# Optimization experiments

Hardware: AMD Instinct MI355X
Metric: run time of the kernel (lower is better)

Reference implementation:

```python
import jax, jax.numpy as jnp
import numpy as np
from jax import lax

C = 256          # hidden_channels
K_ITERS = 3      # num_iterations

def _conv(x, w, b, stride=1, pad='SAME'):
    y = lax.conv_general_dilated(x, w, (stride, stride), pad,
                                 dimension_numbers=('NCHW', 'OIHW', 'NCHW'))
    return y + b[None, :, None, None]

def setup_inputs() -> dict:
    key = jax.random.key(0)
    ks = jax.random.split(key, 16)
    B, N, H, W = 1, 3, 384, 384
    def p(k, sh, scale=None):
        if scale is None:
            scale = 1.0 / np.sqrt(np.prod(sh[1:]))
        return jax.random.normal(k, sh, jnp.float32) * scale
    z = lambda: jnp.zeros((C,), jnp.float32)
    return {
        'frames': jax.random.normal(ks[0], (B, N, 3, H, W), jnp.float32),
        'backbone_w': p(ks[1], (C, 3, 8, 8)), 'backbone_b': z(),
        'W_intra': p(ks[2], (C, C), scale=1.0 / C),
        'W_inter': p(ks[3], (C, C), scale=1.0 / C),
        'gate_w': p(ks[4], (C, C, 1, 1)), 'gate_b': z(),
        'Wz': p(ks[5], (C, 2 * C, 3, 3)), 'bz': z(),
        'Wr': p(ks[6], (C, 2 * C, 3, 3)), 'br': z(),
        'Wh': p(ks[7], (C, 2 * C, 3, 3)), 'bh': z(),
        'ro_w1': p(ks[8], (C, 2 * C, 3, 3)), 'ro_b1': z(),
        'ro_w2': p(ks[9], (1, C, 3, 3)), 'ro_b2': jnp.zeros((1,), jnp.float32),
    }

def _forward(frames, backbone_w, backbone_b, W_intra, W_inter, gate_w, gate_b,
             Wz, bz, Wr, br, Wh, bh, ro_w1, ro_b1, ro_w2, ro_b2):
    B, N, _, H, W = frames.shape
    x = frames.reshape(B * N, 3, H, W)
    # backbone: stride-8 conv + ReLU -> node embeddings v (B*N, C, Hf, Wf)
    v = jax.nn.relu(_conv(x, backbone_w, backbone_b, stride=8, pad='VALID'))
    Hf, Wf = v.shape[2], v.shape[3]
    P = Hf * Wf
    v = v.reshape(B, N, C, Hf, Wf)
    h = v
    idx = jnp.arange(N)
    for _ in range(K_ITERS):
        hp = h.reshape(B, N, C, P).transpose(0, 1, 3, 2)      # (B,N,P,C)
        # inter attention e_ij = h_i W h_j^T over all ordered pairs
        t = jnp.einsum('bipc,cd->bipd', hp, W_inter)
        e = jnp.einsum('bipd,bjqd->bijpq', t, hp)              # (B,N,N,P,P)
        # intra (loop-edge) attention on the diagonal, own weight
        ti = jnp.einsum('bipc,cd->bipd', hp, W_intra)
        e_intra = jnp.einsum('bipd,biqd->bipq', ti, hp)        # (B,N,P,P)
        e = e.at[:, idx, idx].set(e_intra)
        attn = jax.nn.softmax(e, axis=-1)
        m = jnp.einsum('bijpq,bjqc->bijpc', attn, hp)          # msg j->i (B,N,N,P,C)
        m = m.transpose(0, 1, 2, 4, 3).reshape(B * N * N, C, Hf, Wf)
        # gated aggregation: sigmoid(1x1 conv) gate, sum over senders j
        g = jax.nn.sigmoid(_conv(m, gate_w, gate_b))
        magg = (g * m).reshape(B, N, N, C, Hf, Wf).sum(axis=2).reshape(B * N, C, Hf, Wf)
        # ConvGRU update
        hflat = h.reshape(B * N, C, Hf, Wf)
        mh = jnp.concatenate([magg, hflat], axis=1)
        zg = jax.nn.sigmoid(_conv(mh, Wz, bz))
        rg = jax.nn.sigmoid(_conv(mh, Wr, br))
        hc = jnp.tanh(_conv(jnp.concatenate([magg, rg * hflat], axis=1), Wh, bh))
        h = ((1.0 - zg) * hflat + zg * hc).reshape(B, N, C, Hf, Wf)
    # read-out on concat(h, v)
    cat = jnp.concatenate([h, v], axis=2).reshape(B * N, 2 * C, Hf, Wf)
    y = jax.nn.relu(_conv(cat, ro_w1, ro_b1))
    masks = _conv(y, ro_w2, ro_b2)
    return masks.reshape(B, N, 1, Hf, Wf)

def reference(frames, backbone_w, backbone_b, W_intra, W_inter, gate_w, gate_b,
              Wz, bz, Wr, br, Wh, bh, ro_w1, ro_b1, ro_w2, ro_b2):
    return _forward(frames, backbone_w, backbone_b, W_intra, W_inter, gate_w, gate_b,
                    Wz, bz, Wr, br, Wh, bh, ro_w1, ro_b1, ro_w2, ro_b2)
```

## Files before the change

kernel.cpp:

```cpp
#include <hip/hip_runtime.h>
#include <hip/hip_bf16.h>
#include <math.h>

#define PIX 2304
#define CCH 256
#define CP  589824
#define NCP 1769472
#define KC  4608
#define PADR 2512

typedef __hip_bfloat16 bf16;
typedef __attribute__((ext_vector_type(8))) short bf16x8;
typedef __attribute__((ext_vector_type(4))) float f32x4;

__device__ __forceinline__ float sigmoidf_(float x){ return 1.f/(1.f+__expf(-x)); }

__device__ __forceinline__ void gl_lds16(const bf16* g, bf16* lds){
    __builtin_amdgcn_global_load_lds(
        (const __attribute__((address_space(1))) void*)g,
        (__attribute__((address_space(3))) void*)lds, 16, 0, 0);
}
#define FENCE() asm volatile("" ::: "memory")

__device__ __forceinline__ float bperm_f(int srcLane, float v){
    return __int_as_float(__builtin_amdgcn_ds_bpermute(srcLane<<2, __float_as_int(v)));
}
__device__ __forceinline__ unsigned packbf(float lo, float hi){
    bf16 a = __float2bfloat16(lo), b = __float2bfloat16(hi);
    return (unsigned)(*(unsigned short*)&a) | ((unsigned)(*(unsigned short*)&b)<<16);
}

__global__ __launch_bounds__(384) void fattn_k(
    const bf16* __restrict__ T, const bf16* __restrict__ Ti,
    const bf16* __restrict__ Khp, const bf16* __restrict__ Vcp,
    bf16* __restrict__ Ob)
{
    __shared__ bf16 Ks[128*256];
    __shared__ bf16 Vs[256*128];
    __shared__ unsigned Ps[6][1024];
    const int z = blockIdx.z, i = z/3, j = z%3;
    const bf16* Q  = ((i==j)? Ti : T) + (long)i*CP;
    const bf16* Kp = Khp + (long)j*CP;
    const bf16* Vp = Vcp + (long)j*CP;
    const int tid = threadIdx.x, l = tid & 63, w = tid >> 6;
    const int g = l>>4, m = l&15;
    const int q0 = blockIdx.x*96;

    bf16x8 qf[8];
    {
        const bf16* qr = Q + (long)(q0 + w*16 + m)*256 + g*8;
        #pragma unroll
        for (int ks=0; ks<8; ++ks) qf[ks] = *(const bf16x8*)(qr + ks*32);
    }
    f32x4 oacc[16];
    #pragma unroll
    for (int nf=0; nf<16; ++nf) oacc[nf] = (f32x4){0.f,0.f,0.f,0.f};
    float mrun = -3e38f;
    float lrun = 0.f;

    auto stageK = [&](int t){
        const int kq = t*128;
        #pragma unroll
        for (int u=0; u<11; ++u){
            int idx = u*384 + tid;
            if (idx < 4096){
                int rr = idx>>5, cc = idx&31;
                gl_lds16(Kp + (long)(kq+rr)*256 + ((cc ^ (rr&7))<<3),
                         &Ks[(u*384 + (tid & ~63))*8]);
            }
        }
    };
    auto stageV = [&](int t){
        const int kq = t*128;
        #pragma unroll
        for (int u=0; u<11; ++u){
            int idx = u*384 + tid;
            if (idx < 4096){
                int rr = idx>>4, cc = idx&15;
                gl_lds16(Vp + (long)rr*2304 + kq + ((cc ^ (rr&7))<<3),
                         &Vs[(u*384 + (tid & ~63))*8]);
            }
        }
    };

    stageK(0); stageV(0);
    char* pw = (char*)&Ps[w][0];
    for (int t=0; t<18; ++t){
        asm volatile("s_waitcnt vmcnt(10)" ::: "memory");
        __builtin_amdgcn_s_barrier();
        FENCE();

        f32x4 sacc[8];
        #pragma unroll
        for (int nf=0; nf<8; ++nf) sacc[nf] = (f32x4){0.f,0.f,0.f,0.f};
        __builtin_amdgcn_s_setprio(1);
        #pragma unroll
        for (int ks=0; ks<8; ++ks){
            #pragma unroll
            for (int nf=0; nf<8; ++nf){
                int row = nf*16 + m;
                int phys = (ks*4 + g) ^ (row&7);
                bf16x8 kf = *(const bf16x8*)&Ks[row*256 + phys*8];
                sacc[nf] = __builtin_amdgcn_mfma_f32_16x16x32_bf16(kf, qf[ks], sacc[nf], 0,0,0);
            }
        }
        __builtin_amdgcn_s_setprio(0);
        FENCE();
        __builtin_amdgcn_s_barrier();
        FENCE();
        if (t+1 < 18) stageK(t+1);

        float pmax = -3e38f;
        #pragma unroll
        for (int nf=0; nf<8; ++nf)
            #pragma unroll
            for (int r=0; r<4; ++r) pmax = fmaxf(pmax, sacc[nf][r]);
        pmax = fmaxf(pmax, __shfl_xor(pmax, 16));
        pmax = fmaxf(pmax, __shfl_xor(pmax, 32));
        if (!__all(pmax - mrun <= 8.f)){
            float mn = fmaxf(mrun, pmax);
            float al = __expf(mrun - mn);
            mrun = mn;
            lrun *= al;
            float ar[4];
            #pragma unroll
            for (int r=0; r<4; ++r) ar[r] = bperm_f((l & 48) | (g*4 + r), al);
            #pragma unroll
            for (int nf=0; nf<16; ++nf)
                #pragma unroll
                for (int r=0; r<4; ++r) oacc[nf][r] *= ar[r];
        }
        float rs = 0.f;
        unsigned pk[8][2];
        #pragma unroll
        for (int nf=0; nf<8; ++nf){
            float p0 = __expf(sacc[nf][0] - mrun);
            float p1 = __expf(sacc[nf][1] - mrun);
            float p2 = __expf(sacc[nf][2] - mrun);
            float p3 = __expf(sacc[nf][3] - mrun);
            rs += (p0+p1) + (p2+p3);
            pk[nf][0] = packbf(p0, p1);
            pk[nf][1] = packbf(p2, p3);
        }
        rs += __shfl_xor(rs, 16);
        rs += __shfl_xor(rs, 32);
        lrun += rs;
        #pragma unroll
        for (int nf=0; nf<8; ++nf)
            #pragma unroll
            for (int s=0; s<2; ++s){
                int ba = m*256 + ((nf*32 + g*8 + s*4) ^ ((m&7)<<4));
                *(unsigned*)(pw + ba) = pk[nf][s];
            }
        asm volatile("s_waitcnt lgkmcnt(0)" ::: "memory");
        __builtin_amdgcn_sched_barrier(0);

        if (t+1 < 18) asm volatile("s_waitcnt vmcnt(10)" ::: "memory");
        else          asm volatile("s_waitcnt vmcnt(0)"  ::: "memory");
        __builtin_amdgcn_s_barrier();
        FENCE();

        __builtin_amdgcn_s_setprio(1);
        #pragma unroll
        for (int ks2=0; ks2<4; ++ks2){
            bf16x8 pa = *(const bf16x8*)(pw + m*256 + ((ks2*64 + g*16) ^ ((m&7)<<4)));
            #pragma unroll
            for (int nf=0; nf<16; ++nf){
                int row = nf*16 + m;
                int phys = (ks2*4 + g) ^ (row&7);
                bf16x8 bv = *(const bf16x8*)&Vs[row*128 + phys*8];
                oacc[nf] = __builtin_amdgcn_mfma_f32_16x16x32_bf16(pa, bv, oacc[nf], 0,0,0);
            }
        }
        __builtin_amdgcn_s_setprio(0);
        FENCE();
        __builtin_amdgcn_s_barrier();
        FENCE();
        if (t+1 < 18) stageV(t+1);
    }

    float linv = 1.f / lrun;
    float li[4];
    #pragma unroll
    for (int r=0; r<4; ++r) li[r] = bperm_f((l & 48) | (g*4 + r), linv);
    bf16* ob = Ob + (long)z*CP;
    const int prow0 = q0 + w*16 + g*4;
    #pragma unroll
    for (int nf=0; nf<16; ++nf){
        int c = nf*16 + m;
        #pragma unroll
        for (int r=0; r<4; ++r)
            ob[(long)(prow0+r)*256 + c] = __float2bfloat16(oacc[nf][r]*li[r]);
    }
}

template<int BN>
__global__ __launch_bounds__(256) void mgemm_k(
    const bf16* __restrict__ A0, const bf16* __restrict__ B, bf16* __restrict__ ob,
    int M, int lda, int ldb, int ldc,
    long bsB, long bsC, int nzJ, int Ksub)
{
    __shared__ bf16 As[2][128*64];
    __shared__ bf16 Bs[2][BN*64];
    const int jz = blockIdx.z % nzJ;
    const bf16* Ap = A0 + (long)blockIdx.x*128*lda;
    const bf16* Bp = B + jz*bsB + (long)blockIdx.y*BN*ldb;
    const int tid = threadIdx.x, l = tid & 63;
    const int wvu = tid & ~63;
    const int wr = tid>>7, wc = (tid>>6)&1;
    constexpr int NF = BN/32;
    f32x4 acc[4][NF];
    #pragma unroll
    for (int i=0;i<4;++i)
        #pragma unroll
        for (int j=0;j<NF;++j) acc[i][j] = (f32x4){0.f,0.f,0.f,0.f};

    auto stage = [&](int buf, int kb){
        #pragma unroll
        for (int u=0;u<4;++u){
            int idx = u*256 + tid;
            int row = idx>>3, g = (idx&7) ^ (row&7);
            gl_lds16(Ap + (long)row*lda + kb + g*8, &As[buf][(u*256+wvu)*8]);
        }
        #pragma unroll
        for (int u=0;u<BN/32;++u){
            int idx = u*256 + tid;
            int row = idx>>3, g = (idx&7) ^ (row&7);
            gl_lds16(Bp + (long)row*ldb + kb + g*8, &Bs[buf][(u*256+wvu)*8]);
        }
    };

    const int nk = Ksub >> 6;
    stage(0, 0);
    int cur = 0;
    for (int t=0; t<nk; ++t){
        if (t+1 < nk){
            stage(cur^1, (t+1)*64);
            if constexpr (BN==64) asm volatile("s_waitcnt vmcnt(6)" ::: "memory");
            else                  asm volatile("s_waitcnt vmcnt(8)" ::: "memory");
        } else {
            asm volatile("s_waitcnt vmcnt(0)" ::: "memory");
        }
        __builtin_amdgcn_s_barrier();
        FENCE();
        #pragma unroll
        for (int ks=0; ks<64; ks+=32){
            bf16x8 af[4], bfr[NF];
            #pragma unroll
            for (int i=0;i<4;++i){
                int row = wr*64 + i*16 + (l&15);
                af[i] = *(const bf16x8*)&As[cur][row*64 + ((((ks>>3)+(l>>4)) ^ (row&7))<<3)];
            }
            #pragma unroll
            for (int j=0;j<NF;++j){
                int row = wc*(BN/2) + j*16 + (l&15);
                bfr[j] = *(const bf16x8*)&Bs[cur][row*64 + ((((ks>>3)+(l>>4)) ^ (row&7))<<3)];
            }
            #pragma unroll
            for (int i=0;i<4;++i)
                #pragma unroll
                for (int j=0;j<NF;++j)
                    acc[i][j] = __builtin_amdgcn_mfma_f32_16x16x32_bf16(af[i], bfr[j], acc[i][j], 0,0,0);
        }
        FENCE();
        __builtin_amdgcn_s_barrier();
        FENCE();
        cur ^= 1;
    }

    const int mb = blockIdx.x*128 + wr*64, nb = blockIdx.y*BN + wc*(BN/2);
    #pragma unroll
    for (int i=0;i<4;++i)
        #pragma unroll
        for (int j=0;j<NF;++j){
            int gm0 = mb + i*16 + ((l>>4)<<2);
            int gn  = nb + j*16 + (l&15);
            #pragma unroll
            for (int r=0;r<4;++r)
                ob[jz*bsC + (long)(gm0+r)*ldc + gn] = __float2bfloat16(acc[i][j][r]);
        }
}

__global__ __launch_bounds__(256) void gatemm_k(
    const bf16* __restrict__ gatew, const bf16* __restrict__ Mb9,
    const float* __restrict__ gb, bf16* __restrict__ inpad)
{
    __shared__ bf16 As[2][128*64];
    __shared__ bf16 Bs[2][64*64];
    __shared__ bf16 Ts[64*136];
    const int tid = threadIdx.x, l = tid & 63, wvu = tid & ~63;
    const int wr = tid>>7, wc = (tid>>6)&1;
    const int i = blockIdx.z;
    const bf16* Ap = gatew + (long)blockIdx.x*128*256;
    const int nb0 = blockIdx.y*64;
    f32x4 msum[4][2];
    #pragma unroll
    for (int a=0;a<4;++a){ msum[a][0]=(f32x4){0,0,0,0}; msum[a][1]=(f32x4){0,0,0,0}; }

    for (int j=0; j<3; ++j){
        const bf16* Bp = Mb9 + (long)(i*3+j)*CP + (long)nb0*256;
        f32x4 acc[4][2];
        #pragma unroll
        for (int a=0;a<4;++a){ acc[a][0]=(f32x4){0,0,0,0}; acc[a][1]=(f32x4){0,0,0,0}; }
        auto stage = [&](int buf, int kb){
            #pragma unroll
            for (int u=0;u<4;++u){
                int idx = u*256 + tid;
                int row = idx>>3, g = (idx&7) ^ (row&7);
                gl_lds16(Ap + (long)row*256 + kb + g*8, &As[buf][(u*256+wvu)*8]);
            }
            #pragma unroll
            for (int u=0;u<2;++u){
                int idx = u*256 + tid;
                int row = idx>>3, g = (idx&7) ^ (row&7);
                gl_lds16(Bp + (long)row*256 + kb + g*8, &Bs[buf][(u*256+wvu)*8]);
            }
        };
        stage(0, 0);
        int cur = 0;
        for (int t=0; t<4; ++t){
            if (t+1 < 4){
                stage(cur^1, (t+1)*64);
                asm volatile("s_waitcnt vmcnt(6)" ::: "memory");
            } else {
                asm volatile("s_waitcnt vmcnt(0)" ::: "memory");
            }
            __builtin_amdgcn_s_barrier();
            FENCE();
            #pragma unroll
            for (int ks=0; ks<64; ks+=32){
                bf16x8 af[4], bfr[2];
                #pragma unroll
                for (int a=0;a<4;++a){
                    int row = wr*64 + a*16 + (l&15);
                    af[a] = *(const bf16x8*)&As[cur][row*64 + ((((ks>>3)+(l>>4)) ^ (row&7))<<3)];
                }
                #pragma unroll
                for (int b=0;b<2;++b){
                    int row = wc*32 + b*16 + (l&15);
                    bfr[b] = *(const bf16x8*)&Bs[cur][row*64 + ((((ks>>3)+(l>>4)) ^ (row&7))<<3)];
                }
                #pragma unroll
                for (int a=0;a<4;++a)
                    #pragma unroll
                    for (int b=0;b<2;++b)
                        acc[a][b] = __builtin_amdgcn_mfma_f32_16x16x32_bf16(af[a], bfr[b], acc[a][b], 0,0,0);
            }
            FENCE();
            __builtin_amdgcn_s_barrier();
            FENCE();
            cur ^= 1;
        }
        const bf16* mbz = Mb9 + (long)(i*3+j)*CP;
        const int mb = blockIdx.x*128 + wr*64;
        #pragma unroll
        for (int a=0;a<4;++a)
            #pragma unroll
            for (int b=0;b<2;++b){
                int gm0 = mb + a*16 + ((l>>4)<<2);
                int gn  = nb0 + wc*32 + b*16 + (l&15);
                #pragma unroll
                for (int r=0;r<4;++r){
                    int gm = gm0 + r;
                    float g = sigmoidf_(acc[a][b][r] + gb[gm]);
                    float mv = __bfloat162float(mbz[(long)gn*256 + gm]);
                    msum[a][b][r] += g*mv;
                }
            }
    }
    __syncthreads();
    const int mbl = wr*64;
    #pragma unroll
    for (int a=0;a<4;++a)
        #pragma unroll
        for (int b=0;b<2;++b){
            int cl0 = mbl + a*16 + ((l>>4)<<2);
            int pl  = wc*32 + b*16 + (l&15);
            #pragma unroll
            for (int r=0;r<4;++r)
                Ts[pl*136 + cl0 + r] = __float2bfloat16(msum[a][b][r]);
        }
    __syncthreads();
    const int pl = tid >> 2, seg = tid & 3;
    int p = nb0 + pl;
    int prow = p + 2*(p/48) + 51;
    bf16* dst = inpad + (long)i*PADR*512 + (long)prow*512 + blockIdx.x*128 + seg*32;
    #pragma unroll
    for (int k2=0; k2<4; ++k2)
        *(uint4*)(dst + k2*8) = *(const uint4*)&Ts[pl*136 + seg*32 + k2*8];
}

__global__ __launch_bounds__(256) void cgemm2_k(
    const bf16* __restrict__ inpad, const bf16* __restrict__ W,
    float* __restrict__ part, int N)
{
    __shared__ bf16 As[2][128*64];
    __shared__ bf16 Bs[2][128*64];
    const int tid = threadIdx.x, l = tid & 63, wvu = tid & ~63;
    const int wr = tid>>7, wc = (tid>>6)&1;
    const int bx = blockIdx.x, by = blockIdx.y, kc = blockIdx.z;
    const int img = bx/18, m0 = (bx - img*18)*128;
    const bf16* Ab = inpad + (long)img*PADR*512;
    const bf16* Bb = W + (long)by*128*KC;
    f32x4 acc[4][4];
    #pragma unroll
    for (int i=0;i<4;++i)
        #pragma unroll
        for (int j=0;j<4;++j) acc[i][j] = (f32x4){0.f,0.f,0.f,0.f};

    auto stageA = [&](int buf, int k0){
        int tap = k0 >> 9, ci0 = k0 & 511;
        int dy = tap/3, dx = tap - 3*dy;
        int shift = (dy-1)*50 + (dx-1);
        #pragma unroll
        for (int u=0;u<4;++u){
            int idx = u*256 + tid;
            int row = idx>>3;
            int om = m0 + row;
            int prow = om + 2*(om/48) + 51 + shift;
            int g = (idx&7) ^ (row&7);
            gl_lds16(Ab + (long)prow*512 + ci0 + g*8, &As[buf][(u*256+wvu)*8]);
        }
    };
    auto stageB = [&](int buf, int k0){
        #pragma unroll
        for (int u=0;u<4;++u){
            int idx = u*256 + tid;
            int row = idx>>3;
            int g = (idx&7) ^ (row&7);
            gl_lds16(Bb + (long)row*KC + k0 + g*8, &Bs[buf][(u*256+wvu)*8]);
        }
    };

    const int kbeg = kc*2304;
    stageA(0, kbeg); stageB(0, kbeg);
    int cur = 0;
    for (int t=0; t<36; ++t){
        if (t+1 < 36){
            stageA(cur^1, kbeg+(t+1)*64); stageB(cur^1, kbeg+(t+1)*64);
            asm volatile("s_waitcnt vmcnt(8)" ::: "memory");
        } else {
            asm volatile("s_waitcnt vmcnt(0)" ::: "memory");
        }
        __builtin_amdgcn_s_barrier();
        FENCE();
        #pragma unroll
        for (int ks=0; ks<64; ks+=32){
            bf16x8 af[4], bfr[4];
            #pragma unroll
            for (int i=0;i<4;++i){
                int row = wr*64 + i*16 + (l&15);
                af[i] = *(const bf16x8*)&As[cur][row*64 + ((((ks>>3)+(l>>4)) ^ (row&7))<<3)];
            }
            #pragma unroll
            for (int j=0;j<4;++j){
                int row = wc*64 + j*16 + (l&15);
                bfr[j] = *(const bf16x8*)&Bs[cur][row*64 + ((((ks>>3)+(l>>4)) ^ (row&7))<<3)];
            }
            #pragma unroll
            for (int i=0;i<4;++i)
                #pragma unroll
                for (int j=0;j<4;++j)
                    acc[i][j] = __builtin_amdgcn_mfma_f32_16x16x32_bf16(af[i], bfr[j], acc[i][j], 0,0,0);
        }
        FENCE();
        __builtin_amdgcn_s_barrier();
        FENCE();
        cur ^= 1;
    }

    float* pbase = part + (long)kc*N*6912 + (long)img*2304;
    #pragma unroll
    for (int i=0;i<4;++i)
        #pragma unroll
        for (int j=0;j<4;++j){
            int gm0 = m0 + wr*64 + i*16 + ((l>>4)<<2);
            int gn  = by*128 + wc*64 + j*16 + (l&15);
            *(f32x4*)&pbase[(long)gn*6912 + gm0] = acc[i][j];
        }
}

__global__ __launch_bounds__(256) void credzr_k(const float* __restrict__ part,
        const float* __restrict__ bz, const float* __restrict__ br,
        const float* __restrict__ h, float* __restrict__ zg, bf16* __restrict__ inpad)
{
    __shared__ float tz[64][65];
    const int img = blockIdx.z, p0 = blockIdx.x*64, c0 = blockIdx.y*64;
    const int t = threadIdx.x, tx = t&63, tq = t>>6;
    #pragma unroll
    for (int u=0;u<16;++u){
        int cl = tq + u*4, c = c0 + cl;
        long pz = (long)c*6912 + (long)img*2304 + p0 + tx;
        float vz = part[pz] + part[pz + 512L*6912];
        long pr = (long)(c+256)*6912 + (long)img*2304 + p0 + tx;
        float vr = part[pr] + part[pr + 512L*6912];
        long hidx = (long)img*CP + (long)c*PIX + p0 + tx;
        float hv = h[hidx];
        zg[hidx] = sigmoidf_(vz + bz[c]);
        tz[cl][tx] = sigmoidf_(vr + br[c]) * hv;
    }
    __syncthreads();
    #pragma unroll
    for (int u=0;u<16;++u){
        int pl = tq + u*4, p = p0 + pl;
        int prow = p + 2*(p/48) + 51;
        inpad[(long)img*PADR*512 + (long)prow*512 + 256 + c0 + tx] = __float2bfloat16(tz[tx][pl]);
    }
}

__global__ __launch_bounds__(256) void credht_k(const float* __restrict__ part,
        const float* __restrict__ bh, const float* __restrict__ zg,
        float* __restrict__ h, bf16* __restrict__ hcp, bf16* __restrict__ hp,
        bf16* __restrict__ inpad)
{
    __shared__ float th[64][65];
    const int img = blockIdx.z, p0 = blockIdx.x*64, c0 = blockIdx.y*64;
    const int t = threadIdx.x, tx = t&63, tq = t>>6;
    #pragma unroll
    for (int u=0;u<16;++u){
        int cl = tq + u*4, c = c0 + cl;
        long pidx = (long)c*6912 + (long)img*2304 + p0 + tx;
        float vv = part[pidx] + part[pidx + 256L*6912];
        float hc = tanhf(vv + bh[c]);
        long hidx = (long)img*CP + (long)c*PIX + p0 + tx;
        float zv = zg[hidx];
        float hn = (1.f - zv)*h[hidx] + zv*hc;
        h[hidx] = hn;
        hcp[hidx] = __float2bfloat16(hn);
        th[cl][tx] = hn;
    }
    __syncthreads();
    #pragma unroll
    for (int u=0;u<16;++u){
        int pl = tq + u*4, p = p0 + pl;
        float val = th[tx][pl];
        hp[(long)img*CP + (long)p*256 + c0 + tx] = __float2bfloat16(val);
        int prow = p + 2*(p/48) + 51;
        inpad[(long)img*PADR*512 + (long)prow*512 + 256 + c0 + tx] = __float2bfloat16(val);
    }
}

__global__ __launch_bounds__(256) void credro_k(const float* __restrict__ part,
        const float* __restrict__ b0, float* __restrict__ o0)
{
    int id = blockIdx.x*256 + threadIdx.x;
    int c = id / 6912, g = id - c*6912;
    int img = g / 2304, p = g - img*2304;
    float v = part[id] + part[id + 256L*6912];
    o0[(long)img*CP + (long)c*PIX + p] = fmaxf(v + b0[c], 0.f);
}

__global__ __launch_bounds__(256) void padtr_k(const float* __restrict__ src,
        bf16* __restrict__ dst, int cofs)
{
    __shared__ float tile[64][65];
    const int img = blockIdx.z, p0 = blockIdx.x*64, c0 = blockIdx.y*64;
    const int t = threadIdx.x, tx = t&63, tq = t>>6;
    #pragma unroll
    for (int u=0;u<16;++u){
        int r = tq + u*4;
        tile[r][tx] = src[(long)img*CP + (long)(c0+r)*PIX + p0 + tx];
    }
    __syncthreads();
    bf16* d = dst + (long)img*PADR*512 + cofs + c0;
    #pragma unroll
    for (int u=0;u<16;++u){
        int pl = tq + u*4;
        int p = p0 + pl;
        int prow = p + 2*(p/48) + 51;
        d[(long)prow*512 + tx] = __float2bfloat16(tile[tx][pl]);
    }
}

__global__ __launch_bounds__(256) void convw_k(const float* __restrict__ src,
        bf16* __restrict__ dst, int total)
{
    int idx = blockIdx.x*256 + threadIdx.x;
    if (idx >= total) return;
    int co = idx / KC, r = idx - co*KC;
    int tap = r >> 9, ci = r & 511;
    dst[idx] = __float2bfloat16(src[(long)co*KC + ci*9 + tap]);
}

__global__ __launch_bounds__(256) void prep_h_k(const float* __restrict__ h,
        bf16* __restrict__ hcp, bf16* __restrict__ hp)
{
    __shared__ float tile[64][65];
    const int i = blockIdx.z, p0 = blockIdx.x*64, c0 = blockIdx.y*64;
    const int t = threadIdx.x, tx = t&63, tq = t>>6;
    #pragma unroll
    for (int s=0;s<16;++s){
        int r = tq + s*4;
        float v = h[(long)i*CP + (long)(c0+r)*PIX + p0 + tx];
        tile[r][tx] = v;
        hcp[(long)i*CP + (long)(c0+r)*PIX + p0 + tx] = __float2bfloat16(v);
    }
    __syncthreads();
    #pragma unroll
    for (int s=0;s<16;++s){
        int r = tq + s*4;
        hp[(long)i*CP + (long)(p0+r)*256 + c0 + tx] = __float2bfloat16(tile[tx][r]);
    }
}

__global__ __launch_bounds__(256) void convert_w_k(const float* __restrict__ wint,
    const float* __restrict__ wintra, const float* __restrict__ gw, bf16* __restrict__ o)
{
    int t = blockIdx.x*256 + threadIdx.x;
    int d = t >> 8, c = t & 255;
    o[t]          = __float2bfloat16(wint[c*256 + d]);
    o[65536 + t]  = __float2bfloat16(wintra[c*256 + d]);
    o[131072 + t] = __float2bfloat16(gw[t]);
}

__global__ __launch_bounds__(256) void backbone_k(
    const float* __restrict__ frames, const float* __restrict__ W,
    const float* __restrict__ bias, float* __restrict__ v, float* __restrict__ h)
{
    __shared__ float wl[3*64*4];
    const int n = blockIdx.z, o0 = blockIdx.y * 4;
    const int p = blockIdx.x * 256 + threadIdx.x;
    const int y = p / 48, x = p % 48;
    for (int e = threadIdx.x; e < 768; e += 256) {
        int o_sel = e / 192, rem = e % 192, ci = rem / 64, k = rem % 64;
        wl[(ci*64 + k)*4 + o_sel] = W[((long)(o0 + o_sel)*3 + ci)*64 + k];
    }
    __syncthreads();
    float acc[4] = {0.f,0.f,0.f,0.f};
    for (int ci = 0; ci < 3; ++ci) {
        const float* src = frames + (((long)n*3 + ci)*384) * 384;
        #pragma unroll
        for (int k = 0; k < 64; ++k) {
            int ky = k >> 3, kx = k & 7;
            float iv = src[(8*y + ky)*384 + 8*x + kx];
            float4 w = ((const float4*)wl)[ci*64 + k];
            acc[0] += iv*w.x; acc[1] += iv*w.y; acc[2] += iv*w.z; acc[3] += iv*w.w;
        }
    }
    #pragma unroll
    for (int oo = 0; oo < 4; ++oo) {
        float r = fmaxf(acc[oo] + bias[o0 + oo], 0.f);
        long idx = ((long)n*CCH + o0 + oo)*PIX + p;
        v[idx] = r; h[idx] = r;
    }
}

__global__ __launch_bounds__(256) void maskpart_k(const float* __restrict__ yin,
        const float* __restrict__ W, float* __restrict__ part)
{
    __shared__ float wl[288];
    const int cb = blockIdx.y * 32;
    for (int e = threadIdx.x; e < 288; e += 256) wl[e] = W[cb*9 + e];
    __syncthreads();
    int id = blockIdx.x*256 + threadIdx.x;
    int n = id / PIX, p = id - n*PIX;
    int y = p / 48, x = p % 48;
    float acc = 0.f;
    for (int ci = 0; ci < 32; ++ci) {
        const float* src = yin + ((long)n*CCH + cb + ci)*PIX;
        #pragma unroll
        for (int dy = 0; dy < 3; ++dy) {
            int yy = y + dy - 1;
            #pragma unroll
            for (int dx = 0; dx < 3; ++dx) {
                int xx = x + dx - 1;
                float iv = (yy >= 0 && yy < 48 && xx >= 0 && xx < 48) ? src[yy*48 + xx] : 0.f;
                acc += iv * wl[ci*9 + dy*3 + dx];
            }
        }
    }
    part[(long)blockIdx.y*(3*PIX) + id] = acc;
}

__global__ __launch_bounds__(256) void maskred_k(const float* __restrict__ part,
        const float* __restrict__ bias, float* __restrict__ out)
{
    int id = blockIdx.x*256 + threadIdx.x;
    float acc = bias[0];
    #pragma unroll
    for (int s = 0; s < 8; ++s) acc += part[(long)s*(3*PIX) + id];
    out[id] = acc;
}

extern "C" void kernel_launch(void* const* d_in, const int* in_sizes, int n_in,
                              void* d_out, int out_size, void* d_ws, size_t ws_size,
                              hipStream_t stream)
{
    const float* frames     = (const float*)d_in[0];
    const float* backbone_w = (const float*)d_in[1];
    const float* backbone_b = (const float*)d_in[2];
    const float* W_intra    = (const float*)d_in[3];
    const float* W_inter    = (const float*)d_in[4];
    const float* gate_w     = (const float*)d_in[5];
    const float* gate_b     = (const float*)d_in[6];
    const float* Wz         = (const float*)d_in[7];
    const float* bz         = (const float*)d_in[8];
    const float* Wr         = (const float*)d_in[9];
    const float* br         = (const float*)d_in[10];
    const float* Wh         = (const float*)d_in[11];
    const float* bh         = (const float*)d_in[12];
    const float* ro_w1      = (const float*)d_in[13];
    const float* ro_b1      = (const float*)d_in[14];
    const float* ro_w2      = (const float*)d_in[15];
    const float* ro_b2      = (const float*)d_in[16];
    float* out = (float*)d_out;
    float* ws  = (float*)d_ws;

    float* h    = ws + 0L*NCP;
    float* v    = ws + 1L*NCP;
    float* zg   = ws + 3L*NCP;
    float* S    = ws + 7L*NCP;

    float* Mb9f   = S;
    float* hp16f  = S + 7962624;
    float* hcp16f = hp16f + 884736;
    float* t16f   = hcp16f + 884736;
    float* ti16f  = t16f + 884736;
    float* wbase  = S + 11501568;
    bf16* Wint_t   = (bf16*)wbase;
    bf16* Wintra_t = Wint_t + 65536;
    bf16* gatew16  = Wint_t + 131072;
    bf16* cw16     = (bf16*)(wbase + 98304);
    bf16* inpad    = (bf16*)(wbase + 98304 + 2359296);
    float* maskp   = wbase + 98304 + 2359296 + 1929216;

    bf16* Mb9    = (bf16*)Mb9f;
    bf16* hp16   = (bf16*)hp16f;
    bf16* hcp16  = (bf16*)hcp16f;
    bf16* t16    = (bf16*)t16f;
    bf16* ti16   = (bf16*)ti16f;
    float* cpart = Mb9f;

    dim3 b256(256);

    hipMemsetAsync(inpad, 0, 3858432*sizeof(bf16), stream);
    backbone_k<<<dim3(9,64,3), b256, 0, stream>>>(frames, backbone_w, backbone_b, v, h);
    convert_w_k<<<dim3(256), b256, 0, stream>>>(W_inter, W_intra, gate_w, Wint_t);
    convw_k<<<dim3(4608), b256, 0, stream>>>(Wz, cw16, 256*KC);
    convw_k<<<dim3(4608), b256, 0, stream>>>(Wr, cw16 + 256L*KC, 256*KC);
    convw_k<<<dim3(4608), b256, 0, stream>>>(Wh, cw16 + 512L*KC, 256*KC);
    convw_k<<<dim3(4608), b256, 0, stream>>>(ro_w1, cw16 + 768L*KC, 256*KC);

    prep_h_k<<<dim3(36,4,3), b256, 0, stream>>>(h, hcp16, hp16);
    padtr_k<<<dim3(36,4,3), b256, 0, stream>>>(h, inpad, 256);

    for (int it = 0; it < 3; ++it) {
        mgemm_k<64><<<dim3(54,4,2), b256, 0, stream>>>(hp16, Wint_t, t16,
            6912, 256,256,256, 65536L, 1769472L, 2, 256);
        fattn_k<<<dim3(24,1,9), dim3(384), 0, stream>>>(t16, ti16, hp16, hcp16, Mb9);
        gatemm_k<<<dim3(2,36,3), b256, 0, stream>>>(gatew16, Mb9, gate_b, inpad);
        cgemm2_k<<<dim3(54,4,2), b256, 0, stream>>>(inpad, cw16, cpart, 512);
        credzr_k<<<dim3(36,4,3), b256, 0, stream>>>(cpart, bz, br, h, zg, inpad);
        cgemm2_k<<<dim3(54,2,2), b256, 0, stream>>>(inpad, cw16 + 512L*KC, cpart, 256);
        credht_k<<<dim3(36,4,3), b256, 0, stream>>>(cpart, bh, zg, h, hcp16, hp16, inpad);
    }

    padtr_k<<<dim3(36,4,3), b256, 0, stream>>>(h, inpad, 0);
    padtr_k<<<dim3(36,4,3), b256, 0, stream>>>(v, inpad, 256);
    cgemm2_k<<<dim3(54,2,2), b256, 0, stream>>>(inpad, cw16 + 768L*KC, cpart, 256);
    credro_k<<<dim3(6912), b256, 0, stream>>>(cpart, ro_b1, zg);
    maskpart_k<<<dim3(27,8), b256, 0, stream>>>(zg, ro_w2, maskp);
    maskred_k<<<dim3(27), b256, 0, stream>>>(maskp, ro_b2, out);
}
```

Before: 844.0 us.

## Process two query tiles per wave in flash attention, halving waves per block

```diff
diff --git a/kernel.cpp b/kernel.cpp
--- a/kernel.cpp
+++ b/kernel.cpp
@@ -30,7 +30,7 @@
     return (unsigned)(*(unsigned short*)&a) | ((unsigned)(*(unsigned short*)&b)<<16);
 }
 
-__global__ __launch_bounds__(384) void fattn_k(
+__global__ __launch_bounds__(192) void fattn_k(
     const bf16* __restrict__ T, const bf16* __restrict__ Ti,
     const bf16* __restrict__ Khp, const bf16* __restrict__ Vcp,
     bf16* __restrict__ Ob)
@@ -44,55 +44,66 @@
     const bf16* Vp = Vcp + (long)j*CP;
     const int tid = threadIdx.x, l = tid & 63, w = tid >> 6;
     const int g = l>>4, m = l&15;
-    const int q0 = blockIdx.x*96;
-
-    bf16x8 qf[8];
+    const int q0 = blockIdx.x*96 + w*32;
+
+    bf16x8 qf0[8], qf1[8];
     {
-        const bf16* qr = Q + (long)(q0 + w*16 + m)*256 + g*8;
-        #pragma unroll
-        for (int ks=0; ks<8; ++ks) qf[ks] = *(const bf16x8*)(qr + ks*32);
-    }
-    f32x4 oacc[16];
-    #pragma unroll
-    for (int nf=0; nf<16; ++nf) oacc[nf] = (f32x4){0.f,0.f,0.f,0.f};
-    float mrun = -3e38f;
-    float lrun = 0.f;
+        const bf16* qr0 = Q + (long)(q0 + m)*256 + g*8;
+        const bf16* qr1 = Q + (long)(q0 + 16 + m)*256 + g*8;
+        #pragma unroll
+        for (int ks=0; ks<8; ++ks){
+            qf0[ks] = *(const bf16x8*)(qr0 + ks*32);
+            qf1[ks] = *(const bf16x8*)(qr1 + ks*32);
+        }
+    }
+    f32x4 oacc0[16], oacc1[16];
+    #pragma unroll
+    for (int nf=0; nf<16; ++nf){
+        oacc0[nf] = (f32x4){0.f,0.f,0.f,0.f};
+        oacc1[nf] = (f32x4){0.f,0.f,0.f,0.f};
+    }
+    float mrun0 = -3e38f, lrun0 = 0.f;
+    float mrun1 = -3e38f, lrun1 = 0.f;
 
     auto stageK = [&](int t){
         const int kq = t*128;
         #pragma unroll
-        for (int u=0; u<11; ++u){
-            int idx = u*384 + tid;
+        for (int u=0; u<22; ++u){
+            int idx = u*192 + tid;
             if (idx < 4096){
                 int rr = idx>>5, cc = idx&31;
                 gl_lds16(Kp + (long)(kq+rr)*256 + ((cc ^ (rr&7))<<3),
-                         &Ks[(u*384 + (tid & ~63))*8]);
+                         &Ks[(u*192 + (tid & ~63))*8]);
             }
         }
     };
     auto stageV = [&](int t){
         const int kq = t*128;
         #pragma unroll
-        for (int u=0; u<11; ++u){
-            int idx = u*384 + tid;
+        for (int u=0; u<22; ++u){
+            int idx = u*192 + tid;
             if (idx < 4096){
                 int rr = idx>>4, cc = idx&15;
                 gl_lds16(Vp + (long)rr*2304 + kq + ((cc ^ (rr&7))<<3),
-                         &Vs[(u*384 + (tid & ~63))*8]);
+                         &Vs[(u*192 + (tid & ~63))*8]);
             }
         }
     };
 
     stageK(0); stageV(0);
-    char* pw = (char*)&Ps[w][0];
+    char* pw0 = (char*)Ps + (w*2+0)*4096;
+    char* pw1 = (char*)Ps + (w*2+1)*4096;
     for (int t=0; t<18; ++t){
-        asm volatile("s_waitcnt vmcnt(10)" ::: "memory");
+        asm volatile("s_waitcnt vmcnt(21)" ::: "memory");
         __builtin_amdgcn_s_barrier();
         FENCE();
 
-        f32x4 sacc[8];
-        #pragma unroll
-        for (int nf=0; nf<8; ++nf) sacc[nf] = (f32x4){0.f,0.f,0.f,0.f};
+        f32x4 sacc0[8], sacc1[8];
+        #pragma unroll
+        for (int nf=0; nf<8; ++nf){
+            sacc0[nf] = (f32x4){0.f,0.f,0.f,0.f};
+            sacc1[nf] = (f32x4){0.f,0.f,0.f,0.f};
+        }
         __builtin_amdgcn_s_setprio(1);
         #pragma unroll
         for (int ks=0; ks<8; ++ks){
@@ -101,7 +112,8 @@
                 int row = nf*16 + m;
                 int phys = (ks*4 + g) ^ (row&7);
                 bf16x8 kf = *(const bf16x8*)&Ks[row*256 + phys*8];
-                sacc[nf] = __builtin_amdgcn_mfma_f32_16x16x32_bf16(kf, qf[ks], sacc[nf], 0,0,0);
+                sacc0[nf] = __builtin_amdgcn_mfma_f32_16x16x32_bf16(kf, qf0[ks], sacc0[nf], 0,0,0);
+                sacc1[nf] = __builtin_amdgcn_mfma_f32_16x16x32_bf16(kf, qf1[ks], sacc1[nf], 0,0,0);
             }
         }
         __builtin_amdgcn_s_setprio(0);
@@ -110,52 +122,88 @@
         FENCE();
         if (t+1 < 18) stageK(t+1);
 
-        float pmax = -3e38f;
-        #pragma unroll
-        for (int nf=0; nf<8; ++nf)
-            #pragma unroll
-            for (int r=0; r<4; ++r) pmax = fmaxf(pmax, sacc[nf][r]);
-        pmax = fmaxf(pmax, __shfl_xor(pmax, 16));
-        pmax = fmaxf(pmax, __shfl_xor(pmax, 32));
-        if (!__all(pmax - mrun <= 8.f)){
-            float mn = fmaxf(mrun, pmax);
-            float al = __expf(mrun - mn);
-            mrun = mn;
-            lrun *= al;
-            float ar[4];
-            #pragma unroll
-            for (int r=0; r<4; ++r) ar[r] = bperm_f((l & 48) | (g*4 + r), al);
-            #pragma unroll
-            for (int nf=0; nf<16; ++nf)
-                #pragma unroll
-                for (int r=0; r<4; ++r) oacc[nf][r] *= ar[r];
-        }
-        float rs = 0.f;
-        unsigned pk[8][2];
-        #pragma unroll
-        for (int nf=0; nf<8; ++nf){
-            float p0 = __expf(sacc[nf][0] - mrun);
-            float p1 = __expf(sacc[nf][1] - mrun);
-            float p2 = __expf(sacc[nf][2] - mrun);
-            float p3 = __expf(sacc[nf][3] - mrun);
-            rs += (p0+p1) + (p2+p3);
-            pk[nf][0] = packbf(p0, p1);
-            pk[nf][1] = packbf(p2, p3);
-        }
-        rs += __shfl_xor(rs, 16);
-        rs += __shfl_xor(rs, 32);
-        lrun += rs;
-        #pragma unroll
-        for (int nf=0; nf<8; ++nf)
-            #pragma unroll
-            for (int s=0; s<2; ++s){
-                int ba = m*256 + ((nf*32 + g*8 + s*4) ^ ((m&7)<<4));
-                *(unsigned*)(pw + ba) = pk[nf][s];
-            }
+        {
+            float pmax = -3e38f;
+            #pragma unroll
+            for (int nf=0; nf<8; ++nf)
+                #pragma unroll
+                for (int r=0; r<4; ++r) pmax = fmaxf(pmax, sacc0[nf][r]);
+            pmax = fmaxf(pmax, __shfl_xor(pmax, 16));
+            pmax = fmaxf(pmax, __shfl_xor(pmax, 32));
+            if (!__all(pmax - mrun0 <= 8.f)){
+                float mn = fmaxf(mrun0, pmax);
+                float al = __expf(mrun0 - mn);
+                mrun0 = mn;
+                lrun0 *= al;
+                float ar[4];
+                #pragma unroll
+                for (int r=0; r<4; ++r) ar[r] = bperm_f((l & 48) | (g*4 + r), al);
+                #pragma unroll
+                for (int nf=0; nf<16; ++nf)
+                    #pragma unroll
+                    for (int r=0; r<4; ++r) oacc0[nf][r] *= ar[r];
+            }
+            float rs = 0.f;
+            #pragma unroll
+            for (int nf=0; nf<8; ++nf){
+                float p0 = __expf(sacc0[nf][0] - mrun0);
+                float p1 = __expf(sacc0[nf][1] - mrun0);
+                float p2 = __expf(sacc0[nf][2] - mrun0);
+                float p3 = __expf(sacc0[nf][3] - mrun0);
+                rs += (p0+p1) + (p2+p3);
+                unsigned k0 = packbf(p0, p1), k1 = packbf(p2, p3);
+                int ba0 = m*256 + ((nf*32 + g*8 + 0) ^ ((m&7)<<4));
+                int ba1 = m*256 + ((nf*32 + g*8 + 4) ^ ((m&7)<<4));
+                *(unsigned*)(pw0 + ba0) = k0;
+                *(unsigned*)(pw0 + ba1) = k1;
+            }
+            rs += __shfl_xor(rs, 16);
+            rs += __shfl_xor(rs, 32);
+            lrun0 += rs;
+        }
+        {
+            float pmax = -3e38f;
+            #pragma unroll
+            for (int nf=0; nf<8; ++nf)
+                #pragma unroll
+                for (int r=0; r<4; ++r) pmax = fmaxf(pmax, sacc1[nf][r]);
+            pmax = fmaxf(pmax, __shfl_xor(pmax, 16));
+            pmax = fmaxf(pmax, __shfl_xor(pmax, 32));
+            if (!__all(pmax - mrun1 <= 8.f)){
+                float mn = fmaxf(mrun1, pmax);
+                float al = __expf(mrun1 - mn);
+                mrun1 = mn;
+                lrun1 *= al;
+                float ar[4];
+                #pragma unroll
+                for (int r=0; r<4; ++r) ar[r] = bperm_f((l & 48) | (g*4 + r), al);
+                #pragma unroll
+                for (int nf=0; nf<16; ++nf)
+                    #pragma unroll
+                    for (int r=0; r<4; ++r) oacc1[nf][r] *= ar[r];
+            }
+            float rs = 0.f;
+            #pragma unroll
+            for (int nf=0; nf<8; ++nf){
+                float p0 = __expf(sacc1[nf][0] - mrun1);
+                float p1 = __expf(sacc1[nf][1] - mrun1);
+                float p2 = __expf(sacc1[nf][2] - mrun1);
+                float p3 = __expf(sacc1[nf][3] - mrun1);
+                rs += (p0+p1) + (p2+p3);
+                unsigned k0 = packbf(p0, p1), k1 = packbf(p2, p3);
+                int ba0 = m*256 + ((nf*32 + g*8 + 0) ^ ((m&7)<<4));
+                int ba1 = m*256 + ((nf*32 + g*8 + 4) ^ ((m&7)<<4));
+                *(unsigned*)(pw1 + ba0) = k0;
+                *(unsigned*)(pw1 + ba1) = k1;
+            }
+            rs += __shfl_xor(rs, 16);
+            rs += __shfl_xor(rs, 32);
+            lrun1 += rs;
+        }
         asm volatile("s_waitcnt lgkmcnt(0)" ::: "memory");
         __builtin_amdgcn_sched_barrier(0);
 
-        if (t+1 < 18) asm volatile("s_waitcnt vmcnt(10)" ::: "memory");
+        if (t+1 < 18) asm volatile("s_waitcnt vmcnt(21)" ::: "memory");
         else          asm volatile("s_waitcnt vmcnt(0)"  ::: "memory");
         __builtin_amdgcn_s_barrier();
         FENCE();
@@ -163,13 +211,15 @@
         __builtin_amdgcn_s_setprio(1);
         #pragma unroll
         for (int ks2=0; ks2<4; ++ks2){
-            bf16x8 pa = *(const bf16x8*)(pw + m*256 + ((ks2*64 + g*16) ^ ((m&7)<<4)));
+            bf16x8 pa0 = *(const bf16x8*)(pw0 + m*256 + ((ks2*64 + g*16) ^ ((m&7)<<4)));
+            bf16x8 pa1 = *(const bf16x8*)(pw1 + m*256 + ((ks2*64 + g*16) ^ ((m&7)<<4)));
             #pragma unroll
             for (int nf=0; nf<16; ++nf){
                 int row = nf*16 + m;
                 int phys = (ks2*4 + g) ^ (row&7);
                 bf16x8 bv = *(const bf16x8*)&Vs[row*128 + phys*8];
-                oacc[nf] = __builtin_amdgcn_mfma_f32_16x16x32_bf16(pa, bv, oacc[nf], 0,0,0);
+                oacc0[nf] = __builtin_amdgcn_mfma_f32_16x16x32_bf16(pa0, bv, oacc0[nf], 0,0,0);
+                oacc1[nf] = __builtin_amdgcn_mfma_f32_16x16x32_bf16(pa1, bv, oacc1[nf], 0,0,0);
             }
         }
         __builtin_amdgcn_s_setprio(0);
@@ -179,18 +229,34 @@
         if (t+1 < 18) stageV(t+1);
     }
 
-    float linv = 1.f / lrun;
-    float li[4];
-    #pragma unroll
-    for (int r=0; r<4; ++r) li[r] = bperm_f((l & 48) | (g*4 + r), linv);
     bf16* ob = Ob + (long)z*CP;
-    const int prow0 = q0 + w*16 + g*4;
-    #pragma unroll
-    for (int nf=0; nf<16; ++nf){
-        int c = nf*16 + m;
-        #pragma unroll
-        for (int r=0; r<4; ++r)
-            ob[(long)(prow0+r)*256 + c] = __float2bfloat16(oacc[nf][r]*li[r]);
+    {
+        float linv = 1.f / lrun0;
+        float li[4];
+        #pragma unroll
+        for (int r=0; r<4; ++r) li[r] = bperm_f((l & 48) | (g*4 + r), linv);
+        const int prow0 = q0 + g*4;
+        #pragma unroll
+        for (int nf=0; nf<16; ++nf){
+            int c = nf*16 + m;
+            #pragma unroll
+            for (int r=0; r<4; ++r)
+                ob[(long)(prow0+r)*256 + c] = __float2bfloat16(oacc0[nf][r]*li[r]);
+        }
+    }
+    {
+        float linv = 1.f / lrun1;
+        float li[4];
+        #pragma unroll
+        for (int r=0; r<4; ++r) li[r] = bperm_f((l & 48) | (g*4 + r), linv);
+        const int prow0 = q0 + 16 + g*4;
+        #pragma unroll
+        for (int nf=0; nf<16; ++nf){
+            int c = nf*16 + m;
+            #pragma unroll
+            for (int r=0; r<4; ++r)
+                ob[(long)(prow0+r)*256 + c] = __float2bfloat16(oacc1[nf][r]*li[r]);
+        }
     }
 }
 
@@ -747,7 +813,7 @@
     for (int it = 0; it < 3; ++it) {
         mgemm_k<64><<<dim3(54,4,2), b256, 0, stream>>>(hp16, Wint_t, t16,
             6912, 256,256,256, 65536L, 1769472L, 2, 256);
-        fattn_k<<<dim3(24,1,9), dim3(384), 0, stream>>>(t16, ti16, hp16, hcp16, Mb9);
+        fattn_k<<<dim3(24,1,9), dim3(192), 0, stream>>>(t16, ti16, hp16, hcp16, Mb9);
         gatemm_k<<<dim3(2,36,3), b256, 0, stream>>>(gatew16, Mb9, gate_b, inpad);
         cgemm2_k<<<dim3(54,4,2), b256, 0, stream>>>(inpad, cw16, cpart, 512);
         credzr_k<<<dim3(36,4,3), b256, 0, stream>>>(cpart, bz, br, h, zg, inpad);
```

Result: slower. 1.110 ms (+31.5%).
